# Performance work log

Hardware: AMD Instinct MI355X
Metric: run time of the kernel (lower is better)

Reference implementation:

```python
import jax, jax.numpy as jnp
import numpy as np

N, L, C, H, W, HEAD = 16, 256, 512, 32, 32, 16

def setup_inputs() -> dict:
    key = jax.random.key(0)
    ks = jax.random.split(key, 8)
    s = 0.02  # weight init scale
    return {
        "feature": jax.random.normal(ks[0], (N, C, H, W), jnp.float32),
        "token": jax.random.normal(ks[1], (N, L, C), jnp.float32),
        "wq": jax.random.normal(ks[2], (C, C), jnp.float32) * s,
        "bq": jax.random.normal(ks[3], (C,), jnp.float32) * s,
        "wk": jax.random.normal(ks[4], (C, C), jnp.float32) * s,
        "bk": jax.random.normal(ks[5], (C,), jnp.float32) * s,
        "wv": jax.random.normal(ks[6], (C, C), jnp.float32) * s,
        "bv": jax.random.normal(ks[7], (C,), jnp.float32) * s,
    }

def reference(feature, token, wq, bq, wk, bk, wv, bv):
    n, c, hgt, wid = feature.shape
    h = HEAD
    d = c // h
    l = token.shape[1]
    scale = jnp.asarray(np.sqrt(c / h), feature.dtype)
    tok = token.transpose(0, 2, 1)  # (N, C, L)
    # 1x1 conv projections == per-position GEMMs
    v = (jnp.einsum('ncl,dc->ndl', tok, wv) + bv[None, :, None]).reshape(n, h, d, l)
    k = (jnp.einsum('ncl,dc->ndl', tok, wk) + bk[None, :, None]).reshape(n, h, d, l)
    q = (jnp.einsum('nchw,dc->ndhw', feature, wq) + bq[None, :, None, None])
    q = q.reshape(n, h, d, hgt * wid).transpose(0, 1, 3, 2)  # (N, h, HW, d)
    scores = jnp.einsum('nhqd,nhdl->nhql', q, k) / scale  # (N, h, HW, L)
    coef = jax.nn.softmax(scores, axis=-1)
    proj = jnp.einsum('nhdl,nhql->nhdq', v, coef)  # (N, h, d, HW)
    return feature + proj.reshape(n, c, hgt, wid)
```

## Files before the change

### kernel.cpp

```cpp
#include <hip/hip_runtime.h>
#include <hip/hip_bf16.h>

#define N_ 16
#define L_ 256
#define C_ 512
#define HW_ 1024
#define HEADS_ 16
#define DH_ 32

typedef unsigned short u16;
typedef unsigned int u32;
typedef __attribute__((ext_vector_type(8))) short short8_t;
typedef __attribute__((ext_vector_type(4))) float f32x4;

__device__ __forceinline__ u16 f2bs(float f) {
    union { float f; u32 i; } x; x.f = f;
    u32 r = x.i + 0x7fffu + ((x.i >> 16) & 1u);
    return (u16)(r >> 16);
}
__device__ __forceinline__ u32 cvt_pk_bf16(float lo, float hi) {
    u32 r;
    asm("v_cvt_pk_bf16_f32 %0, %1, %2" : "=v"(r) : "v"(lo), "v"(hi));
    return r;
}

__global__ __launch_bounds__(256) void prep_kernel(
    const float* __restrict__ token, const float* __restrict__ wq,
    const float* __restrict__ wk, const float* __restrict__ wv,
    u16* __restrict__ tokb, u16* __restrict__ wqb,
    u16* __restrict__ wkb, u16* __restrict__ wvb)
{
    const int idx = blockIdx.x * 256 + threadIdx.x;
    const float* s; u16* d; int off;
    if (idx < 524288)            { s = token; d = tokb; off = idx; }
    else if (idx < 524288+65536) { s = wq; d = wqb; off = idx - 524288; }
    else if (idx < 524288+131072){ s = wk; d = wkb; off = idx - 524288 - 65536; }
    else                         { s = wv; d = wvb; off = idx - 524288 - 131072; }
    float4 v = ((const float4*)s)[off];
    ushort4 w;
    w.x = f2bs(v.x); w.y = f2bs(v.y); w.z = f2bs(v.z); w.w = f2bs(v.w);
    ((ushort4*)d)[off] = w;
}

__global__ __launch_bounds__(256) void transpose_f_kernel(
    const float* __restrict__ feature, u16* __restrict__ Ft)
{
    __shared__ float LT[64][67];
    const int t = threadIdx.x;
    const int pb = blockIdx.x, cb = blockIdx.y, n = blockIdx.z;
    const int c0 = cb * 64, pos0 = pb * 64;

    #pragma unroll
    for (int r = 0; r < 4; ++r) {
        const int c = r * 16 + (t >> 4);
        const int p = (t & 15) * 4;
        float4 v = *(const float4*)&feature[((size_t)n * C_ + c0 + c) * HW_ + pos0 + p];
        LT[c][p] = v.x; LT[c][p+1] = v.y; LT[c][p+2] = v.z; LT[c][p+3] = v.w;
    }
    __syncthreads();
    #pragma unroll
    for (int rep = 0; rep < 2; ++rep) {
        const int pos = (t >> 3) + rep * 32;
        const int c = (t & 7) * 8;
        u16 tmp[8];
        #pragma unroll
        for (int j = 0; j < 8; ++j) tmp[j] = f2bs(LT[c + j][pos]);
        *(short8_t*)&Ft[(size_t)(n * HW_ + pos0 + pos) * C_ + c0 + c] =
            *(short8_t*)tmp;
    }
}

__global__ __launch_bounds__(256) void gemm_q_kernel(
    const u16* __restrict__ A, const u16* __restrict__ Wb,
    const float* __restrict__ bias, u16* __restrict__ Out)
{
    __shared__ __align__(16) unsigned char smem[16384];
    u16* As = (u16*)smem;
    u16* Bs = (u16*)(smem + 8192);
    u16 (*LTo)[72] = (u16(*)[72])smem;

    const int t = threadIdx.x;
    const int m0 = blockIdx.x * 64, n0 = blockIdx.y * 64;
    const int lane = t & 63, wid = t >> 6;
    const int i16 = lane & 15, g = lane >> 4;
    const int wm = wid >> 1, wn = wid & 1;
    const int row_a = t >> 3, c8 = t & 7;

    f32x4 acc[2][2] = {{{0.f,0.f,0.f,0.f},{0.f,0.f,0.f,0.f}},
                       {{0.f,0.f,0.f,0.f},{0.f,0.f,0.f,0.f}}};
    const float b0 = bias[n0 + wn * 32 + i16];
    const float b1 = bias[n0 + wn * 32 + 16 + i16];

    for (int c0 = 0; c0 < C_; c0 += 64) {
        __syncthreads();
        #pragma unroll
        for (int r = 0; r < 2; ++r) {
            const int m = row_a + r * 32;
            short8_t va = *(const short8_t*)&A[(size_t)(m0 + m) * C_ + c0 + c8 * 8];
            *(short8_t*)&As[m * 64 + ((c8 ^ (m & 7)) << 3)] = va;
            short8_t vb = *(const short8_t*)&Wb[(size_t)(n0 + m) * C_ + c0 + c8 * 8];
            *(short8_t*)&Bs[m * 64 + ((c8 ^ (m & 7)) << 3)] = vb;
        }
        __syncthreads();
        #pragma unroll
        for (int ks = 0; ks < 2; ++ks) {
            short8_t a[2], b[2];
            #pragma unroll
            for (int mt = 0; mt < 2; ++mt) {
                const int m = wm * 32 + mt * 16 + i16;
                a[mt] = *(const short8_t*)&As[m * 64 + ((((ks << 2) | g) ^ (m & 7)) << 3)];
            }
            #pragma unroll
            for (int nt = 0; nt < 2; ++nt) {
                const int d = wn * 32 + nt * 16 + i16;
                b[nt] = *(const short8_t*)&Bs[d * 64 + ((((ks << 2) | g) ^ (d & 7)) << 3)];
            }
            #pragma unroll
            for (int mt = 0; mt < 2; ++mt)
                #pragma unroll
                for (int nt = 0; nt < 2; ++nt)
                    acc[mt][nt] = __builtin_amdgcn_mfma_f32_16x16x32_bf16(
                        a[mt], b[nt], acc[mt][nt], 0, 0, 0);
        }
    }
    __syncthreads();
    #pragma unroll
    for (int mt = 0; mt < 2; ++mt)
        #pragma unroll
        for (int nt = 0; nt < 2; ++nt) {
            const float bb = nt ? b1 : b0;
            #pragma unroll
            for (int r = 0; r < 4; ++r)
                LTo[wm * 32 + mt * 16 + g * 4 + r][wn * 32 + nt * 16 + i16] =
                    f2bs(acc[mt][nt][r] + bb);
        }
    __syncthreads();
    #pragma unroll
    for (int rep = 0; rep < 2; ++rep) {
        const int m = (t >> 3) + rep * 32;
        const int cs = (t & 7) * 8;
        *(short8_t*)&Out[(size_t)(m0 + m) * C_ + n0 + cs] = *(short8_t*)&LTo[m][cs];
    }
}

__global__ __launch_bounds__(256) void gemm_kv_kernel(
    const u16* __restrict__ A, const u16* __restrict__ Wkb,
    const u16* __restrict__ Wvb, const float* __restrict__ bk,
    const float* __restrict__ bv, u16* __restrict__ Kout, u16* __restrict__ Vt)
{
    __shared__ __align__(16) unsigned char smem[24576];
    u16* As  = (u16*)smem;
    u16* Bks = (u16*)(smem + 8192);
    u16* Bvs = (u16*)(smem + 16384);
    u16 (*LTo)[72] = (u16(*)[72])smem;

    const int t = threadIdx.x;
    const int m0 = blockIdx.x * 64, n0 = blockIdx.y * 64;
    const int lane = t & 63, wid = t >> 6;
    const int i16 = lane & 15, g = lane >> 4;
    const int wm = wid >> 1, wn = wid & 1;
    const int row_a = t >> 3, c8 = t & 7;

    f32x4 ak[2][2] = {{{0.f,0.f,0.f,0.f},{0.f,0.f,0.f,0.f}},
                      {{0.f,0.f,0.f,0.f},{0.f,0.f,0.f,0.f}}};
    f32x4 av[2][2] = {{{0.f,0.f,0.f,0.f},{0.f,0.f,0.f,0.f}},
                      {{0.f,0.f,0.f,0.f},{0.f,0.f,0.f,0.f}}};
    const float bk0 = bk[n0 + wn * 32 + i16];
    const float bk1 = bk[n0 + wn * 32 + 16 + i16];
    const float bv0 = bv[n0 + wn * 32 + i16];
    const float bv1 = bv[n0 + wn * 32 + 16 + i16];

    for (int c0 = 0; c0 < C_; c0 += 64) {
        __syncthreads();
        #pragma unroll
        for (int r = 0; r < 2; ++r) {
            const int m = row_a + r * 32;
            const int sw = m * 64 + ((c8 ^ (m & 7)) << 3);
            *(short8_t*)&As[sw]  = *(const short8_t*)&A[(size_t)(m0 + m) * C_ + c0 + c8 * 8];
            *(short8_t*)&Bks[sw] = *(const short8_t*)&Wkb[(size_t)(n0 + m) * C_ + c0 + c8 * 8];
            *(short8_t*)&Bvs[sw] = *(const short8_t*)&Wvb[(size_t)(n0 + m) * C_ + c0 + c8 * 8];
        }
        __syncthreads();
        #pragma unroll
        for (int ks = 0; ks < 2; ++ks) {
            short8_t a[2], bbk[2], bbv[2];
            #pragma unroll
            for (int mt = 0; mt < 2; ++mt) {
                const int m = wm * 32 + mt * 16 + i16;
                a[mt] = *(const short8_t*)&As[m * 64 + ((((ks << 2) | g) ^ (m & 7)) << 3)];
            }
            #pragma unroll
            for (int nt = 0; nt < 2; ++nt) {
                const int d = wn * 32 + nt * 16 + i16;
                const int sw = d * 64 + ((((ks << 2) | g) ^ (d & 7)) << 3);
                bbk[nt] = *(const short8_t*)&Bks[sw];
                bbv[nt] = *(const short8_t*)&Bvs[sw];
            }
            #pragma unroll
            for (int mt = 0; mt < 2; ++mt)
                #pragma unroll
                for (int nt = 0; nt < 2; ++nt) {
                    ak[mt][nt] = __builtin_amdgcn_mfma_f32_16x16x32_bf16(
                        a[mt], bbk[nt], ak[mt][nt], 0, 0, 0);
                    av[mt][nt] = __builtin_amdgcn_mfma_f32_16x16x32_bf16(
                        a[mt], bbv[nt], av[mt][nt], 0, 0, 0);
                }
        }
    }
    const int nb = m0 >> 8, l0 = m0 & 255;
    const size_t vtbase = (size_t)nb * C_ * L_;
    #pragma unroll
    for (int mt = 0; mt < 2; ++mt)
        #pragma unroll
        for (int nt = 0; nt < 2; ++nt) {
            const int d = n0 + wn * 32 + nt * 16 + i16;
            const float bb = nt ? bv1 : bv0;
            ushort4 w;
            w.x = f2bs(av[mt][nt][0] + bb);
            w.y = f2bs(av[mt][nt][1] + bb);
            w.z = f2bs(av[mt][nt][2] + bb);
            w.w = f2bs(av[mt][nt][3] + bb);
            const int l = l0 + wm * 32 + mt * 16 + g * 4;
            *(ushort4*)&Vt[vtbase + (size_t)d * L_ + l] = w;
        }
    __syncthreads();
    #pragma unroll
    for (int mt = 0; mt < 2; ++mt)
        #pragma unroll
        for (int nt = 0; nt < 2; ++nt) {
            const float bb = nt ? bk1 : bk0;
            #pragma unroll
            for (int r = 0; r < 4; ++r)
                LTo[wm * 32 + mt * 16 + g * 4 + r][wn * 32 + nt * 16 + i16] =
                    f2bs(ak[mt][nt][r] + bb);
        }
    __syncthreads();
    #pragma unroll
    for (int rep = 0; rep < 2; ++rep) {
        const int m = (t >> 3) + rep * 32;
        const int cs = (t & 7) * 8;
        *(short8_t*)&Kout[(size_t)(m0 + m) * C_ + n0 + cs] = *(short8_t*)&LTo[m][cs];
    }
}

__global__ __launch_bounds__(256) void attn_kernel(
    const u16* __restrict__ Qws, const u16* __restrict__ Kws,
    const u16* __restrict__ Vws, const float* __restrict__ feature,
    float* __restrict__ out)
{
    __shared__ __align__(16) unsigned char smem[32768];

    const int t = threadIdx.x;
    const int wid = t >> 6, lane = t & 63;
    const int i16 = lane & 15, g = lane >> 4;
    const int pt = blockIdx.x, h = blockIdx.y, n = blockIdx.z;
    const int pos0 = pt * 64;
    const size_t qbase = ((size_t)n * HW_ + pos0) * C_ + h * DH_;
    const size_t kbase = ((size_t)n * L_) * C_ + h * DH_;
    const size_t vbase = (size_t)n * C_ * L_ + (size_t)h * DH_ * L_;

    const int q = wid * 16 + i16;

    short8_t bq = *(const short8_t*)&Qws[qbase + (size_t)q * C_ + g * 8];

    #pragma unroll
    for (int p = 0; p < 4; ++p) {
        const int kr = wid * 64 + p * 16 + (lane >> 2);
        const u16* ksrc = Kws + kbase + (size_t)kr * C_ + (lane & 3) * 8;
        __builtin_amdgcn_global_load_lds(
            (const __attribute__((address_space(1))) void*)ksrc,
            (__attribute__((address_space(3))) void*)(smem + wid * 4096 + p * 1024),
            16, 0, 0);
        const int vd = wid * 8 + p * 2 + (lane >> 5);
        const u16* vsrc = Vws + vbase + (size_t)vd * L_ + ((lane & 31) ^ (vd & 7)) * 8;
        __builtin_amdgcn_global_load_lds(
            (const __attribute__((address_space(1))) void*)vsrc,
            (__attribute__((address_space(3))) void*)(smem + 16384 + wid * 4096 + p * 1024),
            16, 0, 0);
    }
    __syncthreads();

    f32x4 s[16];
    #pragma unroll
    for (int nf = 0; nf < 16; ++nf) {
        short8_t a = *(const short8_t*)(smem + (nf * 16 + i16) * 64 + g * 16);
        f32x4 z = {0.f, 0.f, 0.f, 0.f};
        s[nf] = __builtin_amdgcn_mfma_f32_16x16x32_bf16(a, bq, z, 0, 0, 0);
    }

    float mm[16], sm[16];
    #pragma unroll
    for (int nf = 0; nf < 16; ++nf)
        mm[nf] = fmaxf(fmaxf(s[nf][0], s[nf][1]), fmaxf(s[nf][2], s[nf][3]));
    #pragma unroll
    for (int st = 8; st >= 1; st >>= 1)
        #pragma unroll
        for (int i = 0; i < 8; ++i)
            if (i < st) mm[i] = fmaxf(mm[i], mm[i + st]);
    float m = mm[0];
    m = fmaxf(m, __shfl_xor(m, 16));
    m = fmaxf(m, __shfl_xor(m, 32));

    const float K2 = 0.25506288f;
    #pragma unroll
    for (int nf = 0; nf < 16; ++nf) {
        #pragma unroll
        for (int r = 0; r < 4; ++r) s[nf][r] = exp2f((s[nf][r] - m) * K2);
        sm[nf] = (s[nf][0] + s[nf][1]) + (s[nf][2] + s[nf][3]);
    }
    #pragma unroll
    for (int st = 8; st >= 1; st >>= 1)
        #pragma unroll
        for (int i = 0; i < 8; ++i)
            if (i < st) sm[i] += sm[i + st];
    float ssum = sm[0];
    ssum += __shfl_xor(ssum, 16);
    ssum += __shfl_xor(ssum, 32);
    const float pinv = 1.0f / ssum;

    __syncthreads();

    f32x4 o0 = {0.f, 0.f, 0.f, 0.f}, o1 = {0.f, 0.f, 0.f, 0.f};
    const int e7 = i16 & 7;

    #pragma unroll
    for (int hb = 0; hb < 2; ++hb) {
        #pragma unroll
        for (int nfp = 0; nfp < 8; ++nfp) {
            const int nf = hb * 8 + nfp;
            #pragma unroll
            for (int w = 0; w < 2; ++w) {
                u32 pw = cvt_pk_bf16(s[nf][2 * w] * pinv, s[nf][2 * w + 1] * pinv);
                const int gran = (nfp * 2 + (g >> 1)) ^ e7;
                *(u32*)(smem + q * 256 + gran * 16 + ((g & 1) * 2 + w) * 4) = pw;
            }
        }
        __syncthreads();
        #pragma unroll
        for (int ks = 0; ks < 4; ++ks) {
            short8_t pb = *(const short8_t*)(smem + q * 256 + (((ks * 4 + g) ^ e7) * 16));
            const int vg = (((hb * 4 + ks) * 4 + g) ^ e7) * 16;
            short8_t va0 = *(const short8_t*)(smem + 16384 + i16 * 512 + vg);
            short8_t va1 = *(const short8_t*)(smem + 16384 + (16 + i16) * 512 + vg);
            o0 = __builtin_amdgcn_mfma_f32_16x16x32_bf16(va0, pb, o0, 0, 0, 0);
            o1 = __builtin_amdgcn_mfma_f32_16x16x32_bf16(va1, pb, o1, 0, 0, 0);
        }
        if (hb == 0) __syncthreads();
    }

    const size_t obase = ((size_t)n * C_ + h * DH_) * HW_ + pos0 + q;
    #pragma unroll
    for (int r = 0; r < 4; ++r) {
        const size_t oa = obase + (size_t)(g * 4 + r) * HW_;
        out[oa] = feature[oa] + o0[r];
        const size_t ob = obase + (size_t)(16 + g * 4 + r) * HW_;
        out[ob] = feature[ob] + o1[r];
    }
}

extern "C" void kernel_launch(void* const* d_in, const int* in_sizes, int n_in,
                              void* d_out, int out_size, void* d_ws, size_t ws_size,
                              hipStream_t stream)
{
    const float* feature = (const float*)d_in[0];
    const float* token   = (const float*)d_in[1];
    const float* wq      = (const float*)d_in[2];
    const float* bq      = (const float*)d_in[3];
    const float* wk      = (const float*)d_in[4];
    const float* bk      = (const float*)d_in[5];
    const float* wv      = (const float*)d_in[6];
    const float* bv      = (const float*)d_in[7];
    float* out = (float*)d_out;

    u16* Qws = (u16*)d_ws;
    u16* Kws = Qws + (size_t)N_ * HW_ * C_;
    u16* Vws = Kws + (size_t)N_ * L_ * C_;

    char* ob = (char*)d_out;
    u16* Ft   = (u16*)ob;
    u16* tokb = (u16*)(ob + (16u << 20));
    u16* wqb  = (u16*)(ob + (20u << 20));
    u16* wkb  = (u16*)(ob + (20u << 20) + 524288);
    u16* wvb  = (u16*)(ob + (20u << 20) + 1048576);

    prep_kernel<<<dim3(2816), 256, 0, stream>>>(token, wq, wk, wv,
                                                tokb, wqb, wkb, wvb);
    transpose_f_kernel<<<dim3(16, 8, 16), 256, 0, stream>>>(feature, Ft);
    gemm_q_kernel<<<dim3(256, 8), 256, 0, stream>>>(Ft, wqb, bq, Qws);
    gemm_kv_kernel<<<dim3(64, 8), 256, 0, stream>>>(tokb, wkb, wvb, bk, bv,
                                                    Kws, Vws);
    attn_kernel<<<dim3(16, 16, 16), 256, 0, stream>>>(Qws, Kws, Vws, feature, out);
}
```

Baseline: 80.56 us.

## Fuse feature transpose into Q GEMM using LDS transpose reads, swizzle K loads

Removes the separate transpose kernel by having the Q projection GEMM read fp32 feature directly, convert to bf16, and store it position-major in LDS. The MFMA operand is then fetched with ds_read_b64_tr_b16 transpose reads. This drops one kernel launch and a full bf16 round trip of the feature tensor through global memory. Output is now written directly without staging through LDS, and the operand roles are swapped so weights become A. Separately, K tiles in the attention kernel get an XOR swizzle to reduce LDS bank conflicts, at the cost of extra address arithmetic and an explicit lgkmcnt wait.

```diff
diff --git a/kernel.cpp b/kernel.cpp
--- a/kernel.cpp
+++ b/kernel.cpp
@@ -12,6 +12,7 @@
 typedef unsigned int u32;
 typedef __attribute__((ext_vector_type(8))) short short8_t;
 typedef __attribute__((ext_vector_type(4))) float f32x4;
+typedef __attribute__((ext_vector_type(2))) unsigned int u32x2;
 
 __device__ __forceinline__ u16 f2bs(float f) {
     union { float f; u32 i; } x; x.f = f;
@@ -42,79 +43,70 @@
     ((ushort4*)d)[off] = w;
 }
 
-__global__ __launch_bounds__(256) void transpose_f_kernel(
-    const float* __restrict__ feature, u16* __restrict__ Ft)
-{
-    __shared__ float LT[64][67];
-    const int t = threadIdx.x;
-    const int pb = blockIdx.x, cb = blockIdx.y, n = blockIdx.z;
-    const int c0 = cb * 64, pos0 = pb * 64;
-
-    #pragma unroll
-    for (int r = 0; r < 4; ++r) {
-        const int c = r * 16 + (t >> 4);
-        const int p = (t & 15) * 4;
-        float4 v = *(const float4*)&feature[((size_t)n * C_ + c0 + c) * HW_ + pos0 + p];
-        LT[c][p] = v.x; LT[c][p+1] = v.y; LT[c][p+2] = v.z; LT[c][p+3] = v.w;
-    }
-    __syncthreads();
-    #pragma unroll
-    for (int rep = 0; rep < 2; ++rep) {
-        const int pos = (t >> 3) + rep * 32;
-        const int c = (t & 7) * 8;
-        u16 tmp[8];
-        #pragma unroll
-        for (int j = 0; j < 8; ++j) tmp[j] = f2bs(LT[c + j][pos]);
-        *(short8_t*)&Ft[(size_t)(n * HW_ + pos0 + pos) * C_ + c0 + c] =
-            *(short8_t*)tmp;
-    }
-}
-
-__global__ __launch_bounds__(256) void gemm_q_kernel(
-    const u16* __restrict__ A, const u16* __restrict__ Wb,
+__global__ __launch_bounds__(256) void gemm_qf_kernel(
+    const float* __restrict__ feature, const u16* __restrict__ Wb,
     const float* __restrict__ bias, u16* __restrict__ Out)
 {
     __shared__ __align__(16) unsigned char smem[16384];
     u16* As = (u16*)smem;
     u16* Bs = (u16*)(smem + 8192);
-    u16 (*LTo)[72] = (u16(*)[72])smem;
 
     const int t = threadIdx.x;
     const int m0 = blockIdx.x * 64, n0 = blockIdx.y * 64;
+    const int n = m0 >> 10, pos0 = m0 & (HW_ - 1);
     const int lane = t & 63, wid = t >> 6;
     const int i16 = lane & 15, g = lane >> 4;
     const int wm = wid >> 1, wn = wid & 1;
     const int row_a = t >> 3, c8 = t & 7;
+    const int cst = t >> 2, pq = t & 3;
 
     f32x4 acc[2][2] = {{{0.f,0.f,0.f,0.f},{0.f,0.f,0.f,0.f}},
                        {{0.f,0.f,0.f,0.f},{0.f,0.f,0.f,0.f}}};
-    const float b0 = bias[n0 + wn * 32 + i16];
-    const float b1 = bias[n0 + wn * 32 + 16 + i16];
 
     for (int c0 = 0; c0 < C_; c0 += 64) {
         __syncthreads();
         #pragma unroll
         for (int r = 0; r < 2; ++r) {
             const int m = row_a + r * 32;
-            short8_t va = *(const short8_t*)&A[(size_t)(m0 + m) * C_ + c0 + c8 * 8];
-            *(short8_t*)&As[m * 64 + ((c8 ^ (m & 7)) << 3)] = va;
-            short8_t vb = *(const short8_t*)&Wb[(size_t)(n0 + m) * C_ + c0 + c8 * 8];
-            *(short8_t*)&Bs[m * 64 + ((c8 ^ (m & 7)) << 3)] = vb;
+            *(short8_t*)&As[m * 64 + ((c8 ^ (m & 7)) << 3)] =
+                *(const short8_t*)&Wb[(size_t)(n0 + m) * C_ + c0 + c8 * 8];
+        }
+        #pragma unroll
+        for (int j = 0; j < 4; ++j) {
+            const int pos = j * 16 + pq * 4;
+            float4 v = *(const float4*)&feature[
+                ((size_t)n * C_ + c0 + cst) * HW_ + pos0 + pos];
+            ushort4 w;
+            w.x = f2bs(v.x); w.y = f2bs(v.y); w.z = f2bs(v.z); w.w = f2bs(v.w);
+            *(ushort4*)&Bs[(cst >> 2) * 256 + j * 64 + (cst & 3) * 16 + pq * 4] = w;
         }
         __syncthreads();
         #pragma unroll
         for (int ks = 0; ks < 2; ++ks) {
-            short8_t a[2], b[2];
+            short8_t a[2];
             #pragma unroll
             for (int mt = 0; mt < 2; ++mt) {
                 const int m = wm * 32 + mt * 16 + i16;
                 a[mt] = *(const short8_t*)&As[m * 64 + ((((ks << 2) | g) ^ (m & 7)) << 3)];
             }
+            short8_t b[2];
             #pragma unroll
             for (int nt = 0; nt < 2; ++nt) {
-                const int d = wn * 32 + nt * 16 + i16;
-                b[nt] = *(const short8_t*)&Bs[d * 64 + ((((ks << 2) | g) ^ (d & 7)) << 3)];
-            }
+                const int pb = wn * 2 + nt;
+                const u32 vaddr = 8192 +
+                    (u32)(ks * 32 + g * 8 + pb) * 128 + (u32)i16 * 2;
+                u32x2 lo, hi;
+                asm volatile("ds_read_b64_tr_b16 %0, %1"
+                             : "=v"(lo) : "v"(vaddr));
+                asm volatile("ds_read_b64_tr_b16 %0, %1 offset:512"
+                             : "=v"(hi) : "v"(vaddr));
+                union { u32 w[4]; short8_t v; } pk;
+                pk.w[0] = lo[0]; pk.w[1] = lo[1];
+                pk.w[2] = hi[0]; pk.w[3] = hi[1];
+                b[nt] = pk.v;
+            }
+            asm volatile("s_waitcnt lgkmcnt(0)" ::: "memory");
+            __builtin_amdgcn_sched_barrier(0);
             #pragma unroll
             for (int mt = 0; mt < 2; ++mt)
                 #pragma unroll
@@ -123,23 +115,21 @@
                         a[mt], b[nt], acc[mt][nt], 0, 0, 0);
         }
     }
-    __syncthreads();
-    #pragma unroll
-    for (int mt = 0; mt < 2; ++mt)
+    #pragma unroll
+    for (int mt = 0; mt < 2; ++mt) {
+        const int dbase = wm * 32 + mt * 16 + g * 4;
+        float4 b4 = *(const float4*)&bias[n0 + dbase];
+        const float bb[4] = {b4.x, b4.y, b4.z, b4.w};
         #pragma unroll
         for (int nt = 0; nt < 2; ++nt) {
-            const float bb = nt ? b1 : b0;
-            #pragma unroll
-            for (int r = 0; r < 4; ++r)
-                LTo[wm * 32 + mt * 16 + g * 4 + r][wn * 32 + nt * 16 + i16] =
-                    f2bs(acc[mt][nt][r] + bb);
-        }
-    __syncthreads();
-    #pragma unroll
-    for (int rep = 0; rep < 2; ++rep) {
-        const int m = (t >> 3) + rep * 32;
-        const int cs = (t & 7) * 8;
-        *(short8_t*)&Out[(size_t)(m0 + m) * C_ + n0 + cs] = *(short8_t*)&LTo[m][cs];
+            const int pos = wn * 32 + nt * 16 + i16;
+            ushort4 w;
+            w.x = f2bs(acc[mt][nt][0] + bb[0]);
+            w.y = f2bs(acc[mt][nt][1] + bb[1]);
+            w.z = f2bs(acc[mt][nt][2] + bb[2]);
+            w.w = f2bs(acc[mt][nt][3] + bb[3]);
+            *(ushort4*)&Out[(size_t)(m0 + pos) * C_ + n0 + dbase] = w;
+        }
     }
 }
 
@@ -266,7 +256,8 @@
     #pragma unroll
     for (int p = 0; p < 4; ++p) {
         const int kr = wid * 64 + p * 16 + (lane >> 2);
-        const u16* ksrc = Kws + kbase + (size_t)kr * C_ + (lane & 3) * 8;
+        const int kg = (lane & 3) ^ ((lane >> 3) & 3);
+        const u16* ksrc = Kws + kbase + (size_t)kr * C_ + kg * 8;
         __builtin_amdgcn_global_load_lds(
             (const __attribute__((address_space(1))) void*)ksrc,
             (__attribute__((address_space(3))) void*)(smem + wid * 4096 + p * 1024),
@@ -280,10 +271,11 @@
     }
     __syncthreads();
 
+    const int kgr = g ^ ((i16 >> 1) & 3);
     f32x4 s[16];
     #pragma unroll
     for (int nf = 0; nf < 16; ++nf) {
-        short8_t a = *(const short8_t*)(smem + (nf * 16 + i16) * 64 + g * 16);
+        short8_t a = *(const short8_t*)(smem + (nf * 16 + i16) * 64 + kgr * 16);
         f32x4 z = {0.f, 0.f, 0.f, 0.f};
         s[nf] = __builtin_amdgcn_mfma_f32_16x16x32_bf16(a, bq, z, 0, 0, 0);
     }
@@ -377,7 +369,6 @@
     u16* Vws = Kws + (size_t)N_ * L_ * C_;
 
     char* ob = (char*)d_out;
-    u16* Ft   = (u16*)ob;
     u16* tokb = (u16*)(ob + (16u << 20));
     u16* wqb  = (u16*)(ob + (20u << 20));
     u16* wkb  = (u16*)(ob + (20u << 20) + 524288);
@@ -385,8 +376,7 @@
 
     prep_kernel<<<dim3(2816), 256, 0, stream>>>(token, wq, wk, wv,
                                                 tokb, wqb, wkb, wvb);
-    transpose_f_kernel<<<dim3(16, 8, 16), 256, 0, stream>>>(feature, Ft);
-    gemm_q_kernel<<<dim3(256, 8), 256, 0, stream>>>(Ft, wqb, bq, Qws);
+    gemm_qf_kernel<<<dim3(256, 8), 256, 0, stream>>>(feature, wqb, bq, Qws);
     gemm_kv_kernel<<<dim3(64, 8), 256, 0, stream>>>(tokb, wkb, wvb, bk, bv,
                                                     Kws, Vws);
     attn_kernel<<<dim3(16, 16, 16), 256, 0, stream>>>(Qws, Kws, Vws, feature, out);
```

After: 78.96 us. -2.0%, faster.
